# Kernel optimization log

Measured on AMD Instinct MI355X. Metric: run time of the kernel, lower is better.

The kernel has to match this reference:

```python
import jax, jax.numpy as jnp
import numpy as np

TARGET_TEMP = 0.06
PRED_TEMP = 0.12
N_SK_ITER = 3
SK_EPS = 1e-8
EXP_MAX = 50.0  # exp_max_values[float32]


def setup_inputs() -> dict:
    key = jax.random.key(0)
    k1, k2 = jax.random.split(key)
    B, N, D, K = 8, 1024, 768, 4096
    x = jax.random.normal(k1, (B, N, D), dtype=jnp.float32)
    W = jax.random.normal(k2, (K, D), dtype=jnp.float32)  # torch init normal std=1
    b = jnp.zeros((K,), dtype=jnp.float32)
    return {"x": x, "W": W, "b": b}


def sinkhorn_knopp(M, n_iterations=N_SK_ITER, eps=SK_EPS):
    # stable_exp: shift by max over dim=-2, add EXP_MAX, exponentiate
    shift = jnp.max(M, axis=-2, keepdims=True)
    M = jnp.exp(M + (EXP_MAX - shift))
    for _ in range(n_iterations):
        M = M / (jnp.sum(M, axis=-2, keepdims=True) + eps)
        M = M / (jnp.sum(M, axis=-1, keepdims=True) + eps)
    return M


def reference(x, W, b):
    # F.normalize(x, dim=-1, p=2, eps=1e-7): x / max(||x||, eps)
    nrm = jnp.linalg.norm(x, axis=-1, keepdims=True)
    x_n = x / jnp.maximum(nrm, 1e-7)
    logits = jnp.einsum('bnd,kd->bnk', x_n, W) + b  # [B, N, K]
    # positionwise_sk=True: keep [B, N, K]; sinkhorn over last two dims
    assignments = sinkhorn_knopp(jax.lax.stop_gradient(logits) / TARGET_TEMP)
    K = logits.shape[-1]
    tgt = assignments.reshape(-1, K).astype(jnp.float32)
    pred = logits.reshape(-1, K).astype(jnp.float32)
    loss = -jnp.sum(tgt * jax.nn.log_softmax(pred / PRED_TEMP, axis=-1), axis=-1).mean()
    return (jax.lax.stop_gradient(assignments), loss)
```

## Files before the change

### kernel.cpp

```cpp
#include <hip/hip_runtime.h>
#include <hip/hip_bf16.h>
#include <stdint.h>

#define TT 0.06f
#define PT 0.12f
#define EXPMAX 50.0f
#define SKEPS 1e-8f

typedef __attribute__((ext_vector_type(8))) short short8;
typedef __attribute__((ext_vector_type(4))) float f32x4;

static constexpr int B_ = 8, N_ = 1024, D_ = 768, K_ = 4096;
static constexpr int R_ROWS = B_ * N_;
static constexpr long LOGITS_ELEMS = (long)R_ROWS * K_;
static constexpr int KP = 3 * D_;
static constexpr int CH_ROWS = 16;
static constexpr int NCHUNK = R_ROWS / CH_ROWS;

static constexpr size_t OFF_APACK = 0;
static constexpr size_t OFF_BPACK = OFF_APACK + (size_t)R_ROWS * KP * 2;
static constexpr size_t OFF_PSUM  = OFF_BPACK;
static constexpr size_t OFF_PMAX  = OFF_BPACK + (size_t)K_ * KP * 2;
static constexpr size_t OFF_PSUM0 = OFF_PMAX + (size_t)64 * K_ * 4;
static constexpr size_t OFF_D     = OFF_PSUM0 + (size_t)64 * K_ * 4;
static constexpr size_t OFF_C     = OFF_D + (size_t)B_ * K_ * 4;
static constexpr size_t OFF_R     = OFF_C + (size_t)B_ * K_ * 4;
static constexpr size_t OFF_LSE   = OFF_R + (size_t)R_ROWS * 4;
static constexpr size_t OFF_LOSSP = OFF_LSE + (size_t)R_ROWS * 4;

__device__ __forceinline__ float waveReduceSum(float v) {
#pragma unroll
    for (int m = 1; m < 64; m <<= 1) v += __shfl_xor(v, m, 64);
    return v;
}
__device__ __forceinline__ float waveReduceMax(float v) {
#pragma unroll
    for (int m = 1; m < 64; m <<= 1) v = fmaxf(v, __shfl_xor(v, m, 64));
    return v;
}

__device__ __forceinline__ void gload_lds16(const __hip_bfloat16* g, __hip_bfloat16* l) {
    __builtin_amdgcn_global_load_lds((const __attribute__((address_space(1))) void*)g,
                                     (__attribute__((address_space(3))) void*)l, 16, 0, 0);
}

__global__ __launch_bounds__(256) void k_pack_x(const float* __restrict__ x,
                                                __hip_bfloat16* __restrict__ Ap) {
    int r = blockIdx.x;
    const float* xr = x + (size_t)r * D_;
    int t = threadIdx.x;
    float v0 = xr[t], v1 = xr[t + 256], v2 = xr[t + 512];
    float ss = v0 * v0 + v1 * v1 + v2 * v2;
    ss = waveReduceSum(ss);
    __shared__ float sb[4];
    __shared__ float sscale;
    if ((t & 63) == 0) sb[t >> 6] = ss;
    __syncthreads();
    if (t == 0) {
        float s = sb[0] + sb[1] + sb[2] + sb[3];
        sscale = 1.0f / fmaxf(sqrtf(s), 1e-7f);
    }
    __syncthreads();
    float sc = sscale;
    __hip_bfloat16* ar = Ap + (size_t)r * KP;
    float vv[3] = {v0, v1, v2};
#pragma unroll
    for (int i = 0; i < 3; i++) {
        int d = t + i * 256;
        float xn = vv[i] * sc;
        __hip_bfloat16 hi = __float2bfloat16(xn);
        float lo = xn - __bfloat162float(hi);
        ar[d] = hi;
        ar[768 + d] = hi;
        ar[1536 + d] = __float2bfloat16(lo);
    }
}

__global__ __launch_bounds__(256) void k_pack_w(const float* __restrict__ Wg,
                                                __hip_bfloat16* __restrict__ Bp) {
    int kk = blockIdx.x;
    const float* wr = Wg + (size_t)kk * D_;
    __hip_bfloat16* br = Bp + (size_t)kk * KP;
    int t = threadIdx.x;
#pragma unroll
    for (int i = 0; i < 3; i++) {
        int d = t + i * 256;
        float v = wr[d];
        __hip_bfloat16 hi = __float2bfloat16(v);
        float lo = v - __bfloat162float(hi);
        br[d] = hi;
        br[768 + d] = __float2bfloat16(lo);
        br[1536 + d] = hi;
    }
}

__global__ __launch_bounds__(256) void k_gemm(const __hip_bfloat16* __restrict__ Ap,
                                              const __hip_bfloat16* __restrict__ Bp,
                                              const float* __restrict__ bias,
                                              float* __restrict__ Lg,
                                              float* __restrict__ pmax,
                                              float* __restrict__ psum0) {
    __shared__ __align__(16) __hip_bfloat16 smA[128 * 32];
    __shared__ __align__(16) __hip_bfloat16 smB[128 * 32];
    __shared__ float sm_cmax[4][64];
    __shared__ float sm_csum[4][64];
    __shared__ float sm_bmax[128];
    int t = threadIdx.x;
    int lane = t & 63, w = t >> 6;
    int bn = blockIdx.x, bm = blockIdx.y;
    int wr = (w >> 1) * 64, wc = (w & 1) * 64;
    f32x4 acc[4][4];
#pragma unroll
    for (int i = 0; i < 4; i++)
#pragma unroll
        for (int j = 0; j < 4; j++) acc[i][j] = (f32x4){0.f, 0.f, 0.f, 0.f};

    const __hip_bfloat16* gA0 = Ap + (size_t)(bm * 128 + w * 16 + (lane >> 2)) * KP + (lane & 3) * 8;
    const __hip_bfloat16* gA1 = gA0 + (size_t)64 * KP;
    const __hip_bfloat16* gB0 = Bp + (size_t)(bn * 128 + w * 16 + (lane >> 2)) * KP + (lane & 3) * 8;
    const __hip_bfloat16* gB1 = gB0 + (size_t)64 * KP;
    __hip_bfloat16* lA0 = smA + w * 16 * 32;
    __hip_bfloat16* lA1 = smA + (64 + w * 16) * 32;
    __hip_bfloat16* lB0 = smB + w * 16 * 32;
    __hip_bfloat16* lB1 = smB + (64 + w * 16) * 32;

    int arow = wr + (lane & 15);
    int brow = wc + (lane & 15);
    int kfr = (lane >> 4) * 8;

    for (int kt = 0; kt < KP / 32; ++kt) {
        gload_lds16(gA0, lA0);
        gload_lds16(gA1, lA1);
        gload_lds16(gB0, lB0);
        gload_lds16(gB1, lB1);
        gA0 += 32; gA1 += 32; gB0 += 32; gB1 += 32;
        __syncthreads();
        short8 af[4], bf[4];
#pragma unroll
        for (int i = 0; i < 4; i++) af[i] = *(const short8*)(smA + (arow + i * 16) * 32 + kfr);
#pragma unroll
        for (int j = 0; j < 4; j++) bf[j] = *(const short8*)(smB + (brow + j * 16) * 32 + kfr);
#pragma unroll
        for (int i = 0; i < 4; i++)
#pragma unroll
            for (int j = 0; j < 4; j++)
                acc[i][j] = __builtin_amdgcn_mfma_f32_16x16x32_bf16(af[i], bf[j], acc[i][j], 0, 0, 0);
        __syncthreads();
    }
    int colbase = bn * 128 + wc + (lane & 15);
    int rowbase = bm * 128 + wr + (lane >> 4) * 4;
    float bbv[4];
#pragma unroll
    for (int j = 0; j < 4; j++) {
        int col = colbase + j * 16;
        float bb = bias[col];
        bbv[j] = bb;
        float mx = -3.4e38f;
#pragma unroll
        for (int i = 0; i < 4; i++) {
            int row = rowbase + i * 16;
#pragma unroll
            for (int rr = 0; rr < 4; rr++) {
                float v = acc[i][j][rr] + bb;
                Lg[(size_t)(row + rr) * K_ + col] = v;
                mx = fmaxf(mx, v);
            }
        }
        mx = fmaxf(mx, __shfl_xor(mx, 16, 64));
        mx = fmaxf(mx, __shfl_xor(mx, 32, 64));
        if ((lane >> 4) == 0) sm_cmax[w][j * 16 + (lane & 15)] = mx;
    }
    __syncthreads();
    if (t < 128) {
        int half = t >> 6, ci = t & 63;
        float m = fmaxf(sm_cmax[half][ci], sm_cmax[half + 2][ci]);
        sm_bmax[t] = m;
        pmax[(size_t)bm * K_ + bn * 128 + t] = m;
    }
    __syncthreads();
#pragma unroll
    for (int j = 0; j < 4; j++) {
        int bcol = (w & 1) * 64 + j * 16 + (lane & 15);
        float M = sm_bmax[bcol];
        float s = 0.f;
#pragma unroll
        for (int i = 0; i < 4; i++)
#pragma unroll
            for (int rr = 0; rr < 4; rr++)
                s += __expf((acc[i][j][rr] + bbv[j] - M) * (1.0f / TT));
        s += __shfl_xor(s, 16, 64);
        s += __shfl_xor(s, 32, 64);
        if ((lane >> 4) == 0) sm_csum[w][j * 16 + (lane & 15)] = s;
    }
    __syncthreads();
    if (t < 128) {
        int half = t >> 6, ci = t & 63;
        psum0[(size_t)bm * K_ + bn * 128 + t] = sm_csum[half][ci] + sm_csum[half + 2][ci];
    }
}

__global__ __launch_bounds__(256) void k_prep(const float* __restrict__ pmax,
                                              const float* __restrict__ psum0,
                                              float* __restrict__ Dv,
                                              float* __restrict__ Cc) {
    int i = blockIdx.x * 256 + threadIdx.x;
    int b = i >> 12, k = i & 4095;
    float mv[8];
    float m = -3.4e38f;
#pragma unroll
    for (int nc = 0; nc < 8; nc++) {
        mv[nc] = pmax[(size_t)(b * 8 + nc) * K_ + k];
        m = fmaxf(m, mv[nc]);
    }
    float Dd = EXPMAX - m * (1.0f / TT);
    float S0 = 0.f;
#pragma unroll
    for (int nc = 0; nc < 8; nc++)
        S0 += psum0[(size_t)(b * 8 + nc) * K_ + k] * __expf(mv[nc] * (1.0f / TT) + Dd);
    Dv[i] = Dd;
    Cc[i] = 1.0f / (S0 + SKEPS);
}

template <bool FIRST>
__global__ __launch_bounds__(512) void k_pass(const float* __restrict__ Lg,
                                              const float* __restrict__ Dv,
                                              const float* __restrict__ Cc,
                                              float* __restrict__ Rv,
                                              float* __restrict__ psum,
                                              float* __restrict__ lse) {
    int chunk = blockIdx.x;
    int b = chunk >> 6;
    int t = threadIdx.x;
    int k0 = t * 8;
    const float* Db = Dv + (size_t)b * K_ + k0;
    const float* Cb = Cc + (size_t)b * K_ + k0;
    float Dr[8], Cr[8], acc[8];
#pragma unroll
    for (int j = 0; j < 8; j++) { Dr[j] = Db[j]; Cr[j] = Cb[j]; acc[j] = 0.f; }
    __shared__ float sbS[2][8], sbM[2][8], sb2[2][8];
    int wv = t >> 6;
    for (int rr = 0; rr < CH_ROWS; ++rr) {
        int r = chunk * CH_ROWS + rr;
        const float* row = Lg + (size_t)r * K_;
        f32x4 La = *(const f32x4*)(row + k0);
        f32x4 Lb = *(const f32x4*)(row + k0 + 4);
        float Lv[8] = {La[0], La[1], La[2], La[3], Lb[0], Lb[1], Lb[2], Lb[3]};
        float e[8];
        float dotp = 0.f, mxl = -3.4e38f;
#pragma unroll
        for (int j = 0; j < 8; j++) {
            e[j] = __expf(Lv[j] * (1.0f / TT) + Dr[j]);
            dotp += e[j] * Cr[j];
            if (FIRST) mxl = fmaxf(mxl, Lv[j]);
        }
        dotp = waveReduceSum(dotp);
        if (FIRST) mxl = waveReduceMax(mxl);
        int par = rr & 1;
        if ((t & 63) == 0) {
            sbS[par][wv] = dotp;
            if (FIRST) sbM[par][wv] = mxl;
        }
        __syncthreads();
        float T = 0.f, MX = -3.4e38f;
#pragma unroll
        for (int q = 0; q < 8; q++) {
            T += sbS[par][q];
            if (FIRST) MX = fmaxf(MX, sbM[par][q]);
        }
        float Rprev = FIRST ? 1.0f : Rv[r];
        float Rnew = Rprev / (Rprev * T + SKEPS);
#pragma unroll
        for (int j = 0; j < 8; j++) acc[j] += Rnew * e[j];
        if (t == 0) Rv[r] = Rnew;
        if (FIRST) {
            float mm = MX * (1.0f / PT);
            float s2 = 0.f;
#pragma unroll
            for (int j = 0; j < 8; j++) s2 += __expf(Lv[j] * (1.0f / PT) - mm);
            s2 = waveReduceSum(s2);
            if ((t & 63) == 0) sb2[par][wv] = s2;
            __syncthreads();
            if (t == 0) {
                float S2 = 0.f;
                for (int q = 0; q < 8; q++) S2 += sb2[par][q];
                lse[r] = mm + logf(S2);
            }
        }
    }
    float* ps = psum + (size_t)chunk * K_ + k0;
#pragma unroll
    for (int j = 0; j < 8; j++) ps[j] = acc[j];
}

__global__ __launch_bounds__(256) void k_updC(const float* __restrict__ psum, float* __restrict__ Cc) {
    int i = blockIdx.x * 256 + threadIdx.x;
    int b = i >> 12, k = i & 4095;
    const float* p = psum + (size_t)(b * 64) * K_ + k;
    float s = 0.f;
#pragma unroll 8
    for (int ch = 0; ch < 64; ch++) s += p[(size_t)ch * K_];
    float c = Cc[i];
    Cc[i] = c / (c * s + SKEPS);
}

__global__ __launch_bounds__(512) void k_passF(float* __restrict__ Lg,
                                               const float* __restrict__ Dv,
                                               const float* __restrict__ Cc,
                                               const float* __restrict__ Rv,
                                               const float* __restrict__ lse,
                                               float* __restrict__ lossp) {
    int chunk = blockIdx.x;
    int b = chunk >> 6;
    int t = threadIdx.x;
    int k0 = t * 8;
    const float* Db = Dv + (size_t)b * K_ + k0;
    const float* Cb = Cc + (size_t)b * K_ + k0;
    float Dr[8], Cr[8];
#pragma unroll
    for (int j = 0; j < 8; j++) { Dr[j] = Db[j]; Cr[j] = Cb[j]; }
    __shared__ float sbS[2][8];
    __shared__ float sbL[8];
    int wv = t >> 6;
    float lp = 0.f;
    for (int rr = 0; rr < CH_ROWS; ++rr) {
        int r = chunk * CH_ROWS + rr;
        float* row = Lg + (size_t)r * K_;
        f32x4 La = *(const f32x4*)(row + k0);
        f32x4 Lb = *(const f32x4*)(row + k0 + 4);
        float Lv[8] = {La[0], La[1], La[2], La[3], Lb[0], Lb[1], Lb[2], Lb[3]};
        float e[8];
        float dotp = 0.f;
#pragma unroll
        for (int j = 0; j < 8; j++) {
            e[j] = __expf(Lv[j] * (1.0f / TT) + Dr[j]);
            dotp += e[j] * Cr[j];
        }
        dotp = waveReduceSum(dotp);
        int par = rr & 1;
        if ((t & 63) == 0) sbS[par][wv] = dotp;
        __syncthreads();
        float T = 0.f;
#pragma unroll
        for (int q = 0; q < 8; q++) T += sbS[par][q];
        float Rprev = Rv[r];
        float R2 = Rprev / (Rprev * T + SKEPS);
        float ls = lse[r];
        f32x4 oa, ob;
#pragma unroll
        for (int j = 0; j < 8; j++) {
            float a = R2 * e[j] * Cr[j];
            lp += a * (Lv[j] * (1.0f / PT) - ls);
            if (j < 4) oa[j] = a; else ob[j - 4] = a;
        }
        *(f32x4*)(row + k0) = oa;
        *(f32x4*)(row + k0 + 4) = ob;
    }
    lp = waveReduceSum(lp);
    if ((t & 63) == 0) sbL[wv] = lp;
    __syncthreads();
    if (t == 0) {
        float tot = 0.f;
        for (int q = 0; q < 8; q++) tot += sbL[q];
        lossp[chunk] = tot;
    }
}

__global__ __launch_bounds__(512) void k_loss(const float* __restrict__ lossp, float* __restrict__ out) {
    int t = threadIdx.x;
    float s = lossp[t];
    s = waveReduceSum(s);
    __shared__ float sb[8];
    if ((t & 63) == 0) sb[t >> 6] = s;
    __syncthreads();
    if (t == 0) {
        float tot = 0.f;
        for (int q = 0; q < 8; q++) tot += sb[q];
        out[LOGITS_ELEMS] = -tot / (float)R_ROWS;
    }
}

extern "C" void kernel_launch(void* const* d_in, const int* in_sizes, int n_in,
                              void* d_out, int out_size, void* d_ws, size_t ws_size,
                              hipStream_t stream) {
    const float* x = (const float*)d_in[0];
    const float* W = (const float*)d_in[1];
    const float* bias = (const float*)d_in[2];
    char* ws = (char*)d_ws;
    __hip_bfloat16* Ap = (__hip_bfloat16*)(ws + OFF_APACK);
    __hip_bfloat16* Bp = (__hip_bfloat16*)(ws + OFF_BPACK);
    float* psum = (float*)(ws + OFF_PSUM);
    float* pmax = (float*)(ws + OFF_PMAX);
    float* psum0 = (float*)(ws + OFF_PSUM0);
    float* Dv = (float*)(ws + OFF_D);
    float* Cc = (float*)(ws + OFF_C);
    float* R = (float*)(ws + OFF_R);
    float* lse = (float*)(ws + OFF_LSE);
    float* lossp = (float*)(ws + OFF_LOSSP);
    float* out = (float*)d_out;
    float* Lg = out;

    k_pack_x<<<dim3(R_ROWS), dim3(256), 0, stream>>>(x, Ap);
    k_pack_w<<<dim3(K_), dim3(256), 0, stream>>>(W, Bp);
    k_gemm<<<dim3(K_ / 128, R_ROWS / 128), dim3(256), 0, stream>>>(Ap, Bp, bias, Lg, pmax, psum0);
    k_prep<<<dim3(128), dim3(256), 0, stream>>>(pmax, psum0, Dv, Cc);
    k_pass<true><<<dim3(NCHUNK), dim3(512), 0, stream>>>(Lg, Dv, Cc, R, psum, lse);
    k_updC<<<dim3(128), dim3(256), 0, stream>>>(psum, Cc);
    k_pass<false><<<dim3(NCHUNK), dim3(512), 0, stream>>>(Lg, Dv, Cc, R, psum, lse);
    k_updC<<<dim3(128), dim3(256), 0, stream>>>(psum, Cc);
    k_passF<<<dim3(NCHUNK), dim3(512), 0, stream>>>(Lg, Dv, Cc, R, lse, lossp);
    k_loss<<<dim3(1), dim3(512), 0, stream>>>(lossp, out);
}
```

Before: 466.3 us.

## Rewrite GEMM with 256x256 tiles, double-buffered swizzled LDS and 512 threads

Rewrites the logits GEMM to compute 256x256 output tiles with 8 waves, each wave owning a 128x64 sub-tile. Operands are loaded over a K-step of 64 into double-buffered, XOR-swizzled LDS, so the next tile's global-to-LDS copy overlaps the current tile's MFMAs and LDS bank conflicts drop. It also adds barriers and priority bumps around the MFMA groups. Because the tiles are larger, each block writes half as many column-partial max and sum entries, so the prep kernel now reduces 4 partials per batch instead of 8. The cost is a large dynamic LDS footprint (128 KB), which limits residency to one block per CU, and fewer total blocks.

```diff
diff --git a/kernel.cpp b/kernel.cpp
--- a/kernel.cpp
+++ b/kernel.cpp
@@ -14,6 +14,7 @@
 static constexpr int R_ROWS = B_ * N_;
 static constexpr long LOGITS_ELEMS = (long)R_ROWS * K_;
 static constexpr int KP = 3 * D_;
+static constexpr int NKT = KP / 64;
 static constexpr int CH_ROWS = 16;
 static constexpr int NCHUNK = R_ROWS / CH_ROWS;
 
@@ -94,108 +95,148 @@
     }
 }
 
-__global__ __launch_bounds__(256) void k_gemm(const __hip_bfloat16* __restrict__ Ap,
-                                              const __hip_bfloat16* __restrict__ Bp,
-                                              const float* __restrict__ bias,
-                                              float* __restrict__ Lg,
-                                              float* __restrict__ pmax,
-                                              float* __restrict__ psum0) {
-    __shared__ __align__(16) __hip_bfloat16 smA[128 * 32];
-    __shared__ __align__(16) __hip_bfloat16 smB[128 * 32];
-    __shared__ float sm_cmax[4][64];
-    __shared__ float sm_csum[4][64];
-    __shared__ float sm_bmax[128];
-    int t = threadIdx.x;
-    int lane = t & 63, w = t >> 6;
+__global__ __launch_bounds__(512, 2) void k_gemm(const __hip_bfloat16* __restrict__ Ap,
+                                                 const __hip_bfloat16* __restrict__ Bp,
+                                                 const float* __restrict__ bias,
+                                                 float* __restrict__ Lg,
+                                                 float* __restrict__ pmax,
+                                                 float* __restrict__ psum0) {
+    extern __shared__ __align__(16) char ldsbuf[];
+    __shared__ float sm_cmax[8][64];
+    __shared__ float sm_csum[8][64];
+    __shared__ float sm_bmax[256];
+
+    int tid = threadIdx.x;
+    int lane = tid & 63, w = tid >> 6;
     int bn = blockIdx.x, bm = blockIdx.y;
-    int wr = (w >> 1) * 64, wc = (w & 1) * 64;
-    f32x4 acc[4][4];
-#pragma unroll
-    for (int i = 0; i < 4; i++)
+    int wm = w >> 2, wn = w & 3;
+    int laneM = lane & 15, kq = lane >> 4;
+
+    const __hip_bfloat16* srcA =
+        Ap + (size_t)(bm * 256 + w * 8 + (lane >> 3)) * KP + (((lane & 7) ^ (lane >> 3)) * 8);
+    const __hip_bfloat16* srcB =
+        Bp + (size_t)(bn * 256 + w * 8 + (lane >> 3)) * KP + (((lane & 7) ^ (lane >> 3)) * 8);
+
+    int swz0 = ((kq ^ (lane & 7)) << 4);
+    int aBase = ((wm * 128 + laneM) << 7) + swz0;
+    int bBase = ((wn * 64 + laneM) << 7) + swz0;
+
+    f32x4 acc[8][4];
+#pragma unroll
+    for (int i = 0; i < 8; i++)
 #pragma unroll
         for (int j = 0; j < 4; j++) acc[i][j] = (f32x4){0.f, 0.f, 0.f, 0.f};
 
-    const __hip_bfloat16* gA0 = Ap + (size_t)(bm * 128 + w * 16 + (lane >> 2)) * KP + (lane & 3) * 8;
-    const __hip_bfloat16* gA1 = gA0 + (size_t)64 * KP;
-    const __hip_bfloat16* gB0 = Bp + (size_t)(bn * 128 + w * 16 + (lane >> 2)) * KP + (lane & 3) * 8;
-    const __hip_bfloat16* gB1 = gB0 + (size_t)64 * KP;
-    __hip_bfloat16* lA0 = smA + w * 16 * 32;
-    __hip_bfloat16* lA1 = smA + (64 + w * 16) * 32;
-    __hip_bfloat16* lB0 = smB + w * 16 * 32;
-    __hip_bfloat16* lB1 = smB + (64 + w * 16) * 32;
-
-    int arow = wr + (lane & 15);
-    int brow = wc + (lane & 15);
-    int kfr = (lane >> 4) * 8;
-
-    for (int kt = 0; kt < KP / 32; ++kt) {
-        gload_lds16(gA0, lA0);
-        gload_lds16(gA1, lA1);
-        gload_lds16(gB0, lB0);
-        gload_lds16(gB1, lB1);
-        gA0 += 32; gA1 += 32; gB0 += 32; gB1 += 32;
-        __syncthreads();
-        short8 af[4], bf[4];
-#pragma unroll
-        for (int i = 0; i < 4; i++) af[i] = *(const short8*)(smA + (arow + i * 16) * 32 + kfr);
-#pragma unroll
-        for (int j = 0; j < 4; j++) bf[j] = *(const short8*)(smB + (brow + j * 16) * 32 + kfr);
-#pragma unroll
-        for (int i = 0; i < 4; i++)
-#pragma unroll
-            for (int j = 0; j < 4; j++)
-                acc[i][j] = __builtin_amdgcn_mfma_f32_16x16x32_bf16(af[i], bf[j], acc[i][j], 0, 0, 0);
-        __syncthreads();
-    }
-    int colbase = bn * 128 + wc + (lane & 15);
-    int rowbase = bm * 128 + wr + (lane >> 4) * 4;
+#pragma unroll
+    for (int q = 0; q < 4; ++q) {
+        gload_lds16(srcA + (size_t)q * 64 * KP, (__hip_bfloat16*)(ldsbuf + q * 8192 + w * 1024));
+        gload_lds16(srcB + (size_t)q * 64 * KP, (__hip_bfloat16*)(ldsbuf + 65536 + q * 8192 + w * 1024));
+    }
+    asm volatile("s_waitcnt vmcnt(0)" ::: "memory");
+    __builtin_amdgcn_s_barrier();
+    __builtin_amdgcn_sched_barrier(0);
+
+    int cur = 0;
+    for (int t = 0; t < NKT; ++t) {
+        char* Ab = ldsbuf + cur * 32768;
+        char* Bb = ldsbuf + 65536 + cur * 32768;
+        if (t < NKT - 1) {
+            const __hip_bfloat16* nA = srcA + (size_t)(t + 1) * 64;
+            const __hip_bfloat16* nB = srcB + (size_t)(t + 1) * 64;
+            char* dA = ldsbuf + (cur ^ 1) * 32768;
+            char* dB = ldsbuf + 65536 + (cur ^ 1) * 32768;
+#pragma unroll
+            for (int q = 0; q < 4; ++q) {
+                gload_lds16(nA + (size_t)q * 64 * KP, (__hip_bfloat16*)(dA + q * 8192 + w * 1024));
+                gload_lds16(nB + (size_t)q * 64 * KP, (__hip_bfloat16*)(dB + q * 8192 + w * 1024));
+            }
+        }
+        short8 bf[4][2];
+#pragma unroll
+        for (int j = 0; j < 4; ++j)
+#pragma unroll
+            for (int s = 0; s < 2; ++s)
+                bf[j][s] = *(const short8*)(Bb + ((bBase + j * 2048) ^ (s << 6)));
+#pragma unroll
+        for (int p = 0; p < 4; ++p) {
+            short8 af[2][2];
+#pragma unroll
+            for (int ii = 0; ii < 2; ++ii)
+#pragma unroll
+                for (int s = 0; s < 2; ++s)
+                    af[ii][s] = *(const short8*)(Ab + ((aBase + (p * 2 + ii) * 2048) ^ (s << 6)));
+            __builtin_amdgcn_s_barrier();
+            __builtin_amdgcn_sched_barrier(0);
+            __builtin_amdgcn_s_setprio(1);
+#pragma unroll
+            for (int ii = 0; ii < 2; ++ii)
+#pragma unroll
+                for (int j = 0; j < 4; ++j)
+#pragma unroll
+                    for (int s = 0; s < 2; ++s)
+                        acc[p * 2 + ii][j] = __builtin_amdgcn_mfma_f32_16x16x32_bf16(
+                            af[ii][s], bf[j][s], acc[p * 2 + ii][j], 0, 0, 0);
+            __builtin_amdgcn_s_setprio(0);
+            __builtin_amdgcn_sched_barrier(0);
+            if (p < 3) {
+                __builtin_amdgcn_s_barrier();
+                __builtin_amdgcn_sched_barrier(0);
+            }
+        }
+        asm volatile("s_waitcnt vmcnt(0)" ::: "memory");
+        __builtin_amdgcn_s_barrier();
+        __builtin_amdgcn_sched_barrier(0);
+        cur ^= 1;
+    }
+
+    int colg0 = bn * 256 + wn * 64;
+    int rowg0 = bm * 256 + wm * 128;
     float bbv[4];
 #pragma unroll
-    for (int j = 0; j < 4; j++) {
-        int col = colbase + j * 16;
-        float bb = bias[col];
+    for (int j = 0; j < 4; ++j) {
+        int colg = colg0 + j * 16 + laneM;
+        float bb = bias[colg];
         bbv[j] = bb;
         float mx = -3.4e38f;
 #pragma unroll
-        for (int i = 0; i < 4; i++) {
-            int row = rowbase + i * 16;
-#pragma unroll
-            for (int rr = 0; rr < 4; rr++) {
+        for (int i = 0; i < 8; ++i) {
+            int rowg = rowg0 + i * 16 + kq * 4;
+#pragma unroll
+            for (int rr = 0; rr < 4; ++rr) {
                 float v = acc[i][j][rr] + bb;
-                Lg[(size_t)(row + rr) * K_ + col] = v;
+                Lg[(size_t)(rowg + rr) * K_ + colg] = v;
                 mx = fmaxf(mx, v);
             }
         }
         mx = fmaxf(mx, __shfl_xor(mx, 16, 64));
         mx = fmaxf(mx, __shfl_xor(mx, 32, 64));
-        if ((lane >> 4) == 0) sm_cmax[w][j * 16 + (lane & 15)] = mx;
-    }
-    __syncthreads();
-    if (t < 128) {
-        int half = t >> 6, ci = t & 63;
-        float m = fmaxf(sm_cmax[half][ci], sm_cmax[half + 2][ci]);
-        sm_bmax[t] = m;
-        pmax[(size_t)bm * K_ + bn * 128 + t] = m;
-    }
-    __syncthreads();
-#pragma unroll
-    for (int j = 0; j < 4; j++) {
-        int bcol = (w & 1) * 64 + j * 16 + (lane & 15);
-        float M = sm_bmax[bcol];
+        if (kq == 0) sm_cmax[w][j * 16 + laneM] = mx;
+    }
+    __syncthreads();
+    if (tid < 256) {
+        int wn_t = tid >> 6, ci = tid & 63;
+        float m = fmaxf(sm_cmax[wn_t][ci], sm_cmax[wn_t + 4][ci]);
+        sm_bmax[tid] = m;
+        pmax[(size_t)bm * K_ + bn * 256 + tid] = m;
+    }
+    __syncthreads();
+#pragma unroll
+    for (int j = 0; j < 4; ++j) {
+        float M = sm_bmax[wn * 64 + j * 16 + laneM];
         float s = 0.f;
 #pragma unroll
-        for (int i = 0; i < 4; i++)
-#pragma unroll
-            for (int rr = 0; rr < 4; rr++)
+        for (int i = 0; i < 8; ++i)
+#pragma unroll
+            for (int rr = 0; rr < 4; ++rr)
                 s += __expf((acc[i][j][rr] + bbv[j] - M) * (1.0f / TT));
         s += __shfl_xor(s, 16, 64);
         s += __shfl_xor(s, 32, 64);
-        if ((lane >> 4) == 0) sm_csum[w][j * 16 + (lane & 15)] = s;
-    }
-    __syncthreads();
-    if (t < 128) {
-        int half = t >> 6, ci = t & 63;
-        psum0[(size_t)bm * K_ + bn * 128 + t] = sm_csum[half][ci] + sm_csum[half + 2][ci];
+        if (kq == 0) sm_csum[w][j * 16 + laneM] = s;
+    }
+    __syncthreads();
+    if (tid < 256) {
+        int wn_t = tid >> 6, ci = tid & 63;
+        psum0[(size_t)bm * K_ + bn * 256 + tid] = sm_csum[wn_t][ci] + sm_csum[wn_t + 4][ci];
     }
 }
 
@@ -205,18 +246,18 @@
                                               float* __restrict__ Cc) {
     int i = blockIdx.x * 256 + threadIdx.x;
     int b = i >> 12, k = i & 4095;
-    float mv[8];
+    float mv[4];
     float m = -3.4e38f;
 #pragma unroll
-    for (int nc = 0; nc < 8; nc++) {
-        mv[nc] = pmax[(size_t)(b * 8 + nc) * K_ + k];
+    for (int nc = 0; nc < 4; nc++) {
+        mv[nc] = pmax[(size_t)(b * 4 + nc) * K_ + k];
         m = fmaxf(m, mv[nc]);
     }
     float Dd = EXPMAX - m * (1.0f / TT);
     float S0 = 0.f;
 #pragma unroll
-    for (int nc = 0; nc < 8; nc++)
-        S0 += psum0[(size_t)(b * 8 + nc) * K_ + k] * __expf(mv[nc] * (1.0f / TT) + Dd);
+    for (int nc = 0; nc < 4; nc++)
+        S0 += psum0[(size_t)(b * 4 + nc) * K_ + k] * __expf(mv[nc] * (1.0f / TT) + Dd);
     Dv[i] = Dd;
     Cc[i] = 1.0f / (S0 + SKEPS);
 }
@@ -399,9 +440,11 @@
     float* out = (float*)d_out;
     float* Lg = out;
 
+    hipFuncSetAttribute((const void*)k_gemm, hipFuncAttributeMaxDynamicSharedMemorySize, 131072);
+
     k_pack_x<<<dim3(R_ROWS), dim3(256), 0, stream>>>(x, Ap);
     k_pack_w<<<dim3(K_), dim3(256), 0, stream>>>(W, Bp);
-    k_gemm<<<dim3(K_ / 128, R_ROWS / 128), dim3(256), 0, stream>>>(Ap, Bp, bias, Lg, pmax, psum0);
+    k_gemm<<<dim3(K_ / 256, R_ROWS / 256), dim3(512), 131072, stream>>>(Ap, Bp, bias, Lg, pmax, psum0);
     k_prep<<<dim3(128), dim3(256), 0, stream>>>(pmax, psum0, Dv, Cc);
     k_pass<true><<<dim3(NCHUNK), dim3(512), 0, stream>>>(Lg, Dv, Cc, R, psum, lse);
     k_updC<<<dim3(128), dim3(256), 0, stream>>>(psum, Cc);
```

Result: faster. 418.3 us (-10.3%).
